# Optimization experiments

Measured on AMD Instinct MI355X. Metric: run time of the kernel, lower is better.

The kernel has to match this reference:

```python
import jax, jax.numpy as jnp
import numpy as np

B, DIN, DOUT, GRID_SIZE, SPLINE_ORDER, N_LAYERS = 4096, 1024, 1024, 8, 3, 2
COEFFS = GRID_SIZE + SPLINE_ORDER  # 11


def _kaiming_uniform(key, shape, fan_in):
    # torch nn.init.kaiming_uniform_ default: a=0 -> gain=sqrt(2), bound=sqrt(3)*gain/sqrt(fan_in)
    bound = float(np.sqrt(6.0 / fan_in))
    return jax.random.uniform(key, shape, jnp.float32, -bound, bound)


def setup_inputs() -> dict:
    key = jax.random.key(0)
    ks = jax.random.split(key, 1 + 3 * N_LAYERS)
    x = jax.random.normal(ks[0], (B, DIN), dtype=jnp.float32)
    # knot grid: arange(-so, gs+so+1)*h + lo, h=(hi-lo)/gs  -> shape [GRID_SIZE+2*SPLINE_ORDER+1]
    h = 2.0 / GRID_SIZE
    grid = jnp.arange(-SPLINE_ORDER, GRID_SIZE + SPLINE_ORDER + 1, dtype=jnp.float32) * h - 1.0
    base_w, spline_w, scaler = [], [], []
    for i in range(N_LAYERS):
        base_w.append(_kaiming_uniform(ks[1 + 3 * i], (DOUT, DIN), DIN))
        spline_w.append(_kaiming_uniform(ks[2 + 3 * i], (DOUT, DIN, COEFFS), DIN * COEFFS))
        scaler.append(_kaiming_uniform(ks[3 + 3 * i], (DOUT, DIN), DIN))
    return {
        "x": x,
        "base_w": jnp.stack(base_w),      # [L, DOUT, DIN]
        "spline_w": jnp.stack(spline_w),  # [L, DOUT, DIN, COEFFS]
        "scaler": jnp.stack(scaler),      # [L, DOUT, DIN]
        "grid": grid,                      # [G]
        "spline_order": SPLINE_ORDER,
    }


def b_splines(x, grid, spline_order):
    # x: (B, DIN) -> bases: (B, DIN, COEFFS) via Cox-de Boor recursion
    x = x[..., None]  # (B, DIN, 1)
    bases = ((x >= grid[:-1]) & (x < grid[1:])).astype(x.dtype)  # order-0 indicators
    for k in range(1, spline_order + 1):
        left = (x - grid[: -(k + 1)]) / (grid[k:-1] - grid[: -(k + 1)])
        right = (grid[k + 1:] - x) / (grid[k + 1:] - grid[1:-k])
        bases = left * bases[..., :-1] + right * bases[..., 1:]
    return bases


def reference(x, base_w, spline_w, scaler, grid, spline_order):
    so = int(spline_order)
    n_layers = base_w.shape[0]
    for i in range(n_layers):
        x = jax.nn.silu(x)                                  # base_activation applied before both branches
        base_out = x @ base_w[i].T                          # (B, DOUT)
        bs = b_splines(x, grid, so)                         # (B, DIN, COEFFS)
        w = spline_w[i] * scaler[i][..., None]              # (DOUT, DIN, COEFFS)
        spline_out = jnp.einsum("bic,oic->bo", bs, w)      # == F.linear on flattened (DIN*COEFFS)
        x = base_out + spline_out
    return x
```

## Files before the change

### kernel.cpp

```cpp
#include <hip/hip_runtime.h>
#include <stdint.h>

#define BATCH 4096
#define DIN 1024
#define DOUT 1024
#define NC 11
#define KD 12288
#define NKNOTS 15

typedef __bf16 bf16x8 __attribute__((ext_vector_type(8)));
typedef float f32x4 __attribute__((ext_vector_type(4)));

__device__ __forceinline__ unsigned short f2bf(float f) {
    unsigned int u = __float_as_uint(f);
    unsigned int r = (u + 0x7FFFu + ((u >> 16) & 1u)) >> 16;
    return (unsigned short)r;
}

__global__ __launch_bounds__(256) void build_A(
    const float* __restrict__ x, const float* __restrict__ grid,
    unsigned short* __restrict__ A) {
    __shared__ __align__(16) unsigned short lbs[256 * NC];
    const int tid = threadIdx.x;
    const int b  = blockIdx.x >> 2;
    const int i0 = (blockIdx.x & 3) * 256;
    const int i  = i0 + tid;

    float g[NKNOTS];
#pragma unroll
    for (int j = 0; j < NKNOTS; ++j) g[j] = grid[j];

    const float xv = x[(size_t)b * DIN + i];
    const float s  = xv / (1.f + __expf(-xv));

    float bs[14];
#pragma unroll
    for (int c = 0; c < 14; ++c) bs[c] = (s >= g[c] && s < g[c + 1]) ? 1.f : 0.f;
#pragma unroll
    for (int k = 1; k <= 3; ++k) {
        const float inv = (k == 1) ? 4.f : (k == 2) ? 2.f : (4.f / 3.f);
#pragma unroll
        for (int c = 0; c < 14 - k; ++c) {
            float left  = (s - g[c]) * inv;
            float right = (g[c + k + 1] - s) * inv;
            bs[c] = left * bs[c] + right * bs[c + 1];
        }
    }

    A[(size_t)b * KD + i] = f2bf(s);
#pragma unroll
    for (int c = 0; c < NC; ++c) lbs[tid * NC + c] = f2bf(bs[c]);
    __syncthreads();

    const uint4* src = (const uint4*)lbs;
    uint4* dst = (uint4*)(A + (size_t)b * KD + DIN + (size_t)i0 * NC);
    for (int j = tid; j < 352; j += 256) dst[j] = src[j];
}

__global__ __launch_bounds__(256) void build_W(
    const float* __restrict__ base_w, const float* __restrict__ spline_w,
    const float* __restrict__ scaler, unsigned short* __restrict__ W) {
    __shared__ __align__(16) unsigned short lw[256 * NC];
    const int tid = threadIdx.x;
    const int o  = blockIdx.x >> 2;
    const int i0 = (blockIdx.x & 3) * 256;
    const int i  = i0 + tid;
    const size_t oi = (size_t)o * DIN + i;

    const float sc = scaler[oi];
    W[(size_t)o * KD + i] = f2bf(base_w[oi]);
    const float* sw = spline_w + oi * NC;
#pragma unroll
    for (int c = 0; c < NC; ++c) lw[tid * NC + c] = f2bf(sw[c] * sc);
    __syncthreads();

    const uint4* src = (const uint4*)lw;
    uint4* dst = (uint4*)(W + (size_t)o * KD + DIN + (size_t)i0 * NC);
    for (int j = tid; j < 352; j += 256) dst[j] = src[j];
}

#define BM 256
#define BN 256
#define BK 64

__global__ __launch_bounds__(512, 2) void gemm_kan(
    const unsigned short* __restrict__ A,
    const unsigned short* __restrict__ W,
    float* __restrict__ C, float* __restrict__ Part,
    int kspl, int ktper) {
    __shared__ unsigned short As[2][BM * BK];
    __shared__ unsigned short Bs[2][BN * BK];

    const int tid  = threadIdx.x;
    const int wave = tid >> 6;
    const int lane = tid & 63;
    const int n0  = (blockIdx.x & 3) * BN;
    const int ksp = (blockIdx.x >> 2) % kspl;
    const int m0  = (blockIdx.x / (4 * kspl)) * BM;
    const int wm = wave >> 2;
    const int wn = wave & 3;

    const int srow = lane >> 3;
    const int scol = 8 * ((lane & 7) ^ (lane >> 3));
    const int kbase = ksp * ktper * BK;

    f32x4 acc[8][4];
#pragma unroll
    for (int a = 0; a < 8; ++a)
#pragma unroll
        for (int b = 0; b < 4; ++b) acc[a][b] = (f32x4){0.f, 0.f, 0.f, 0.f};

    auto stage = [&](int kt) {
        const int buf = kt & 1;
        const int kk = kbase + kt * BK + scol;
#pragma unroll
        for (int c = 0; c < 4; ++c) {
            const int chunk = wave * 4 + c;
            const unsigned short* ga = A + (size_t)(m0 + chunk * 8 + srow) * KD + kk;
            __builtin_amdgcn_global_load_lds(
                (const __attribute__((address_space(1))) unsigned int*)ga,
                (__attribute__((address_space(3))) unsigned int*)&As[buf][chunk * 512],
                16, 0, 0);
            const unsigned short* gb = W + (size_t)(n0 + chunk * 8 + srow) * KD + kk;
            __builtin_amdgcn_global_load_lds(
                (const __attribute__((address_space(1))) unsigned int*)gb,
                (__attribute__((address_space(3))) unsigned int*)&Bs[buf][chunk * 512],
                16, 0, 0);
        }
    };

    stage(0);

    const int arow = wm * 128 + (lane & 15);
    const int brow = wn * 64 + (lane & 15);
    const int xr   = lane & 7;
    const int kcol = lane >> 4;

    for (int kt = 0; kt < ktper; ++kt) {
        asm volatile("s_waitcnt vmcnt(0)" ::: "memory");
        __builtin_amdgcn_sched_barrier(0);
        __builtin_amdgcn_s_barrier();
        __builtin_amdgcn_sched_barrier(0);
        if (kt + 1 < ktper) stage(kt + 1);
        __builtin_amdgcn_sched_barrier(0);

        const int cur = kt & 1;
        __builtin_amdgcn_s_setprio(1);
#pragma unroll
        for (int ks = 0; ks < 2; ++ks) {
            const int slot = ((ks * 4 + kcol) ^ xr) * 8;
            bf16x8 af[8], bfr[4];
#pragma unroll
            for (int fm = 0; fm < 8; ++fm)
                af[fm] = *(const bf16x8*)&As[cur][(arow + fm * 16) * BK + slot];
#pragma unroll
            for (int fn = 0; fn < 4; ++fn)
                bfr[fn] = *(const bf16x8*)&Bs[cur][(brow + fn * 16) * BK + slot];
#pragma unroll
            for (int fm = 0; fm < 8; ++fm)
#pragma unroll
                for (int fn = 0; fn < 4; ++fn)
                    acc[fm][fn] = __builtin_amdgcn_mfma_f32_16x16x32_bf16(
                        af[fm], bfr[fn], acc[fm][fn], 0, 0, 0);
        }
        __builtin_amdgcn_s_setprio(0);
    }

    float* Cp = (ksp == 0) ? C : (Part + (size_t)(ksp - 1) * BATCH * DOUT);
    const int crow = (lane >> 4) * 4;
    const int ccol = lane & 15;
#pragma unroll
    for (int fm = 0; fm < 8; ++fm)
#pragma unroll
        for (int fn = 0; fn < 4; ++fn) {
            const int row = m0 + wm * 128 + fm * 16 + crow;
            const int col = n0 + wn * 64 + fn * 16 + ccol;
#pragma unroll
            for (int r = 0; r < 4; ++r)
                Cp[(size_t)(row + r) * DOUT + col] = acc[fm][fn][r];
        }
}

__global__ __launch_bounds__(256) void reduce_add(
    const float* __restrict__ P, float* __restrict__ X, int np) {
    const size_t i = ((size_t)blockIdx.x * 256 + threadIdx.x) * 4;
    f32x4 a = *(const f32x4*)(X + i);
    for (int p = 0; p < np; ++p)
        a = a + *(const f32x4*)(P + (size_t)p * BATCH * DOUT + i);
    *(f32x4*)(X + i) = a;
}

extern "C" void kernel_launch(void* const* d_in, const int* in_sizes, int n_in,
                              void* d_out, int out_size, void* d_ws, size_t ws_size,
                              hipStream_t stream) {
    const float* x        = (const float*)d_in[0];
    const float* base_w   = (const float*)d_in[1];
    const float* spline_w = (const float*)d_in[2];
    const float* scaler   = (const float*)d_in[3];
    const float* grid     = (const float*)d_in[4];
    float* out = (float*)d_out;

    char* ws = (char*)d_ws;
    unsigned short* Abf = (unsigned short*)ws;
    unsigned short* Wbf = (unsigned short*)(ws + 100663296);
    float* xtmp = (float*)(ws + 100663296 + 25165824);
    float* Part = (float*)(ws + 100663296 + 25165824 + 16777216);

    const size_t base_need = 100663296u + 25165824u + 16777216u;
    const int kspl = (ws_size >= base_need + 3u * 16777216u) ? 4 : 2;
    const int ktper = (KD / BK) / kspl;

    for (int layer = 0; layer < 2; ++layer) {
        const float* xin = (layer == 0) ? x : xtmp;
        float* xout      = (layer == 0) ? xtmp : out;
        build_W<<<4096, 256, 0, stream>>>(base_w + (size_t)layer * DOUT * DIN,
                                          spline_w + (size_t)layer * DOUT * DIN * NC,
                                          scaler + (size_t)layer * DOUT * DIN, Wbf);
        build_A<<<16384, 256, 0, stream>>>(xin, grid, Abf);
        gemm_kan<<<64 * kspl, 512, 0, stream>>>(Abf, Wbf, xout, Part, kspl, ktper);
        reduce_add<<<BATCH * DOUT / 1024, 256, 0, stream>>>(Part, xout, kspl - 1);
    }
}
```

Baseline: 333.5 us.

## Fuse split-K reduction into next layer's build_A and pipeline GEMM in half-tiles

The split-K partial sums of layer 0 are now added inside the next layer's build_A, so one reduce_add launch and its read/write of the activation are dropped; only the final layer keeps a reduce pass. The GEMM main loop is split into four 128x128 quadrant steps, each staging half of the next K tile with partial vmcnt waits, so global-to-LDS loads overlap MFMA work. The block index mapping also changes so consecutive blocks share the same N tile for L2 reuse. In exchange the loop carries two barriers per K step and more complex wait-count bookkeeping.

```diff
diff --git a/kernel.cpp b/kernel.cpp
--- a/kernel.cpp
+++ b/kernel.cpp
@@ -18,8 +18,8 @@
 }
 
 __global__ __launch_bounds__(256) void build_A(
-    const float* __restrict__ x, const float* __restrict__ grid,
-    unsigned short* __restrict__ A) {
+    const float* __restrict__ x, const float* __restrict__ P, int np,
+    const float* __restrict__ grid, unsigned short* __restrict__ A) {
     __shared__ __align__(16) unsigned short lbs[256 * NC];
     const int tid = threadIdx.x;
     const int b  = blockIdx.x >> 2;
@@ -30,8 +30,10 @@
 #pragma unroll
     for (int j = 0; j < NKNOTS; ++j) g[j] = grid[j];
 
-    const float xv = x[(size_t)b * DIN + i];
-    const float s  = xv / (1.f + __expf(-xv));
+    float xv = x[(size_t)b * DIN + i];
+    for (int p = 0; p < np; ++p)
+        xv += P[(size_t)p * BATCH * DIN + (size_t)b * DIN + i];
+    const float s = xv / (1.f + __expf(-xv));
 
     float bs[14];
 #pragma unroll
@@ -83,20 +85,51 @@
 #define BN 256
 #define BK 64
 
+#define LOADAF(AF, BASE)                                                       \
+    _Pragma("unroll")                                                          \
+    for (int fm = 0; fm < 4; ++fm)                                             \
+        _Pragma("unroll")                                                      \
+        for (int ks = 0; ks < 2; ++ks)                                         \
+            AF[fm][ks] = *(const bf16x8*)&(BASE)[(wm * 64 + fm * 16 + rof) * 64 + \
+                                                 (((ks * 4 + kcol) ^ xr) * 8)];
+
+#define LOADBF(BF, BASE)                                                       \
+    _Pragma("unroll")                                                          \
+    for (int fn = 0; fn < 2; ++fn)                                             \
+        _Pragma("unroll")                                                      \
+        for (int ks = 0; ks < 2; ++ks)                                         \
+            BF[fn][ks] = *(const bf16x8*)&(BASE)[(wn * 32 + fn * 16 + rof) * 64 + \
+                                                 (((ks * 4 + kcol) ^ xr) * 8)];
+
+#define MFMA16(AF, BF, RO, CO)                                                 \
+    __builtin_amdgcn_s_setprio(1);                                             \
+    _Pragma("unroll")                                                          \
+    for (int ks = 0; ks < 2; ++ks)                                             \
+        _Pragma("unroll")                                                      \
+        for (int fm = 0; fm < 4; ++fm)                                         \
+            _Pragma("unroll")                                                  \
+            for (int fn = 0; fn < 2; ++fn)                                     \
+                acc[(RO) + fm][(CO) + fn] =                                    \
+                    __builtin_amdgcn_mfma_f32_16x16x32_bf16(                   \
+                        AF[fm][ks], BF[fn][ks], acc[(RO) + fm][(CO) + fn], 0, 0, 0); \
+    __builtin_amdgcn_s_setprio(0);
+
 __global__ __launch_bounds__(512, 2) void gemm_kan(
     const unsigned short* __restrict__ A,
     const unsigned short* __restrict__ W,
     float* __restrict__ C, float* __restrict__ Part,
     int kspl, int ktper) {
-    __shared__ unsigned short As[2][BM * BK];
-    __shared__ unsigned short Bs[2][BN * BK];
+    __shared__ unsigned short As[2 * 2 * 8192];
+    __shared__ unsigned short Bs[2 * 2 * 8192];
 
     const int tid  = threadIdx.x;
     const int wave = tid >> 6;
     const int lane = tid & 63;
-    const int n0  = (blockIdx.x & 3) * BN;
-    const int ksp = (blockIdx.x >> 2) % kspl;
-    const int m0  = (blockIdx.x / (4 * kspl)) * BM;
+    const int per = 16 * kspl;
+    const int n0  = (blockIdx.x / per) * BN;
+    const int r   = blockIdx.x % per;
+    const int ksp = r % kspl;
+    const int m0  = (r / kspl) * BM;
     const int wm = wave >> 2;
     const int wn = wave & 3;
 
@@ -110,75 +143,95 @@
 #pragma unroll
         for (int b = 0; b < 4; ++b) acc[a][b] = (f32x4){0.f, 0.f, 0.f, 0.f};
 
-    auto stage = [&](int kt) {
-        const int buf = kt & 1;
+    auto stageA = [&](int buf, int h, int kt) {
         const int kk = kbase + kt * BK + scol;
 #pragma unroll
-        for (int c = 0; c < 4; ++c) {
-            const int chunk = wave * 4 + c;
-            const unsigned short* ga = A + (size_t)(m0 + chunk * 8 + srow) * KD + kk;
+        for (int c = 0; c < 2; ++c) {
+            const int chunk = wave * 2 + c;
+            const unsigned short* ga =
+                A + (size_t)(m0 + h * 128 + chunk * 8 + srow) * KD + kk;
             __builtin_amdgcn_global_load_lds(
                 (const __attribute__((address_space(1))) unsigned int*)ga,
-                (__attribute__((address_space(3))) unsigned int*)&As[buf][chunk * 512],
-                16, 0, 0);
-            const unsigned short* gb = W + (size_t)(n0 + chunk * 8 + srow) * KD + kk;
+                (__attribute__((address_space(3))) unsigned int*)
+                    &As[buf * 16384 + h * 8192 + chunk * 512], 16, 0, 0);
+        }
+    };
+    auto stageB = [&](int buf, int h, int kt) {
+        const int kk = kbase + kt * BK + scol;
+#pragma unroll
+        for (int c = 0; c < 2; ++c) {
+            const int chunk = wave * 2 + c;
+            const unsigned short* gb =
+                W + (size_t)(n0 + h * 128 + chunk * 8 + srow) * KD + kk;
             __builtin_amdgcn_global_load_lds(
                 (const __attribute__((address_space(1))) unsigned int*)gb,
-                (__attribute__((address_space(3))) unsigned int*)&Bs[buf][chunk * 512],
-                16, 0, 0);
+                (__attribute__((address_space(3))) unsigned int*)
+                    &Bs[buf * 16384 + h * 8192 + chunk * 512], 16, 0, 0);
         }
     };
 
-    stage(0);
-
-    const int arow = wm * 128 + (lane & 15);
-    const int brow = wn * 64 + (lane & 15);
+    stageB(0, 0, 0); stageB(0, 1, 0); stageA(0, 0, 0); stageA(0, 1, 0);
+
+    const int rof  = lane & 15;
     const int xr   = lane & 7;
     const int kcol = lane >> 4;
 
-    for (int kt = 0; kt < ktper; ++kt) {
-        asm volatile("s_waitcnt vmcnt(0)" ::: "memory");
+    for (int t = 0; t < ktper; ++t) {
+        const int cur = t & 1;
+        const int nxt = cur ^ 1;
+        const bool pf = (t + 1 < ktper);
+
+        asm volatile("s_waitcnt vmcnt(2)" ::: "memory");
         __builtin_amdgcn_sched_barrier(0);
         __builtin_amdgcn_s_barrier();
         __builtin_amdgcn_sched_barrier(0);
-        if (kt + 1 < ktper) stage(kt + 1);
-        __builtin_amdgcn_sched_barrier(0);
-
-        const int cur = kt & 1;
-        __builtin_amdgcn_s_setprio(1);
-#pragma unroll
-        for (int ks = 0; ks < 2; ++ks) {
-            const int slot = ((ks * 4 + kcol) ^ xr) * 8;
-            bf16x8 af[8], bfr[4];
-#pragma unroll
-            for (int fm = 0; fm < 8; ++fm)
-                af[fm] = *(const bf16x8*)&As[cur][(arow + fm * 16) * BK + slot];
-#pragma unroll
-            for (int fn = 0; fn < 4; ++fn)
-                bfr[fn] = *(const bf16x8*)&Bs[cur][(brow + fn * 16) * BK + slot];
-#pragma unroll
-            for (int fm = 0; fm < 8; ++fm)
-#pragma unroll
-                for (int fn = 0; fn < 4; ++fn)
-                    acc[fm][fn] = __builtin_amdgcn_mfma_f32_16x16x32_bf16(
-                        af[fm], bfr[fn], acc[fm][fn], 0, 0, 0);
-        }
-        __builtin_amdgcn_s_setprio(0);
+
+        const unsigned short* Ab = &As[cur * 16384];
+        const unsigned short* Bb = &Bs[cur * 16384];
+        bf16x8 af[4][2], bf[2][2];
+
+        if (pf) stageB(nxt, 0, t + 1);
+        LOADAF(af, Ab);
+        LOADBF(bf, Bb);
+        MFMA16(af, bf, 0, 0);
+
+        if (pf) stageB(nxt, 1, t + 1);
+        LOADBF(bf, Bb + 8192);
+        MFMA16(af, bf, 0, 2);
+
+        if (pf) { asm volatile("s_waitcnt vmcnt(4)" ::: "memory"); }
+        else    { asm volatile("s_waitcnt vmcnt(0)" ::: "memory"); }
+        __builtin_amdgcn_sched_barrier(0);
+        __builtin_amdgcn_s_barrier();
+        __builtin_amdgcn_sched_barrier(0);
+
+        if (pf) stageA(nxt, 0, t + 1);
+        LOADAF(af, Ab + 8192);
+        MFMA16(af, bf, 4, 2);
+
+        if (pf) stageA(nxt, 1, t + 1);
+        LOADBF(bf, Bb);
+        MFMA16(af, bf, 4, 0);
     }
 
     float* Cp = (ksp == 0) ? C : (Part + (size_t)(ksp - 1) * BATCH * DOUT);
     const int crow = (lane >> 4) * 4;
     const int ccol = lane & 15;
 #pragma unroll
-    for (int fm = 0; fm < 8; ++fm)
-#pragma unroll
-        for (int fn = 0; fn < 4; ++fn) {
-            const int row = m0 + wm * 128 + fm * 16 + crow;
-            const int col = n0 + wn * 64 + fn * 16 + ccol;
-#pragma unroll
-            for (int r = 0; r < 4; ++r)
-                Cp[(size_t)(row + r) * DOUT + col] = acc[fm][fn][r];
-        }
+    for (int H = 0; H < 2; ++H)
+#pragma unroll
+        for (int fm = 0; fm < 4; ++fm)
+#pragma unroll
+            for (int F = 0; F < 2; ++F)
+#pragma unroll
+                for (int fn = 0; fn < 2; ++fn) {
+                    const int row = m0 + H * 128 + wm * 64 + fm * 16 + crow;
+                    const int col = n0 + F * 128 + wn * 32 + fn * 16 + ccol;
+#pragma unroll
+                    for (int rr = 0; rr < 4; ++rr)
+                        Cp[(size_t)(row + rr) * DOUT + col] =
+                            acc[H * 4 + fm][F * 2 + fn][rr];
+                }
 }
 
 __global__ __launch_bounds__(256) void reduce_add(
@@ -216,8 +269,9 @@
         build_W<<<4096, 256, 0, stream>>>(base_w + (size_t)layer * DOUT * DIN,
                                           spline_w + (size_t)layer * DOUT * DIN * NC,
                                           scaler + (size_t)layer * DOUT * DIN, Wbf);
-        build_A<<<16384, 256, 0, stream>>>(xin, grid, Abf);
+        build_A<<<16384, 256, 0, stream>>>(xin, Part, (layer == 0) ? 0 : kspl - 1,
+                                           grid, Abf);
         gemm_kan<<<64 * kspl, 512, 0, stream>>>(Abf, Wbf, xout, Part, kspl, ktper);
-        reduce_add<<<BATCH * DOUT / 1024, 256, 0, stream>>>(Part, xout, kspl - 1);
     }
-}
+    reduce_add<<<BATCH * DOUT / 1024, 256, 0, stream>>>(Part, out, kspl - 1);
+}
```

Result: slower. 369.8 us (+10.9%).
